# Performance work log

Measured on AMD Instinct MI355X. Metric: run time of the kernel, lower is better.

Reference implementation:

```python
import jax, jax.numpy as jnp
import numpy as np
from jax import lax

NAN_CONV_THRESH = 0.5  # stand-in for os.environ['NAN_CONV_THRESH']
DN = ('NCHW', 'OIHW', 'NCHW')


def nan_conv2d(x, w, stride, padding, groups, thresh):
    """NaN-aware conv: NaN inputs are treated as 0 in the contraction; any
    output window whose NaN fraction exceeds `thresh` is skipped (output NaN)."""
    mask = jnp.isnan(x)
    xf = jnp.where(mask, 0.0, x)
    out = lax.conv_general_dilated(
        xf, w, window_strides=(stride, stride),
        padding=[(padding, padding), (padding, padding)],
        feature_group_count=groups, dimension_numbers=DN)
    cout, cin_g, kh, kw = w.shape
    # per-group NaN count via a ones-kernel conv over the mask
    ones_k = jnp.ones((groups, cin_g, kh, kw), dtype=x.dtype)
    cnt = lax.conv_general_dilated(
        mask.astype(x.dtype), ones_k, window_strides=(stride, stride),
        padding=[(padding, padding), (padding, padding)],
        feature_group_count=groups, dimension_numbers=DN)  # [B, groups, H', W']
    frac = cnt / (cin_g * kh * kw)
    frac = jnp.repeat(frac, cout // groups, axis=1)  # broadcast group frac to out channels
    return jnp.where(frac > thresh, jnp.nan, out)


def setup_inputs() -> dict:
    key = jax.random.key(0)
    k1, k2, k3 = jax.random.split(key, 3)
    B, C, H, W = 4, 128, 256, 256
    Cout, K = 256, 3
    x = jax.random.normal(k1, (B, C, H, W), dtype=jnp.float32)
    w_dw = jax.random.normal(k2, (C, 1, K, K), dtype=jnp.float32) / np.sqrt(K * K)
    w_pw = jax.random.normal(k3, (Cout, C, 1, 1), dtype=jnp.float32) / np.sqrt(C)
    return {"x": x, "w_dw": w_dw, "w_pw": w_pw}


def reference(x, w_dw, w_pw):
    C = x.shape[1]
    y = nan_conv2d(x, w_dw, stride=1, padding=1, groups=C, thresh=NAN_CONV_THRESH)  # depthwise
    y = nan_conv2d(y, w_pw, stride=1, padding=0, groups=1, thresh=NAN_CONV_THRESH)  # pointwise 1x1
    return y
```

## Files before the change

### kernel.cpp

```cpp
#include <hip/hip_runtime.h>
#include <hip/hip_bf16.h>

typedef __attribute__((ext_vector_type(8))) short bf16x8;
typedef __attribute__((ext_vector_type(4))) float f32x4;

#define B    4
#define CIN  128
#define COUT 256
#define H    256
#define W    256
#define HW   (H * W)
#define ROWS 8
#define PXW  64

__device__ __forceinline__ unsigned short f2bf(float f) {
  unsigned int u = __builtin_bit_cast(unsigned int, f);
  u += 0x7fff + ((u >> 16) & 1);
  return (unsigned short)(u >> 16);
}

__global__ void cvt_wpw(const float* __restrict__ w, unsigned short* __restrict__ o) {
  int i = blockIdx.x * 256 + threadIdx.x;
  if (i < COUT * CIN) o[i] = f2bf(w[i]);
}

struct Row { float L; f32x4 a; f32x4 b; float R; };

__device__ __forceinline__ float rget(const Row& r, int j) {
  return (j < 0) ? r.L : (j < 4) ? r.a[j & 3] : (j < 8) ? r.b[j & 3] : r.R;
}

__device__ __forceinline__ Row load_row(const float* xr, int px0, bool pL, bool pR) {
  Row r;
  r.a = *(const f32x4*)(xr + px0);
  r.b = *(const f32x4*)(xr + px0 + 4);
  r.L = pL ? xr[px0 - 1] : 0.f;
  r.R = pR ? xr[px0 + 8] : 0.f;
  return r;
}

__device__ __forceinline__ Row zero_row() {
  Row r; r.L = r.R = 0.f;
  r.a = (f32x4){0.f,0.f,0.f,0.f};
  r.b = (f32x4){0.f,0.f,0.f,0.f};
  return r;
}

__device__ __forceinline__ unsigned swz(unsigned La) {
  unsigned g = ((La >> 8) & 7) ^ ((La >> 11) & 7);
  return La ^ (g << 4);
}

__global__ __launch_bounds__(1024, 4) void fused_kernel(
    const float* __restrict__ x, const float* __restrict__ wdw,
    const unsigned short* __restrict__ wb, float* __restrict__ out)
{
  int bid = blockIdx.x;
  int xcd = bid & 7;
  int k   = bid >> 3;
  int hcl = k & 3;
  int s   = (k >> 2) & 3;
  int b   = k >> 4;
  int hc  = xcd * 4 + hcl;
  int hBase = hc * ROWS;

  int t = threadIdx.x;
  int ci  = t >> 3;
  int pxg = t & 7;
  int px0 = s * PXW + pxg * 8;
  bool pL = px0 > 0, pR = px0 + 8 < W;

  __shared__ __align__(16) char yb[ROWS * PXW * CIN * 2];

  float wr[9];
#pragma unroll
  for (int q = 0; q < 9; ++q) wr[q] = wdw[ci * 9 + q];

  const float* xc = x + ((size_t)b * CIN + ci) * HW;

  Row A  = (hBase > 0) ? load_row(xc + (size_t)(hBase - 1) * W, px0, pL, pR) : zero_row();
  Row Bv = load_row(xc + (size_t)hBase * W, px0, pL, pR);
  Row C  = load_row(xc + (size_t)(hBase + 1) * W, px0, pL, pR);

#pragma unroll
  for (int r = 0; r < ROWS; ++r) {
    Row D;
    if (r < ROWS - 1) {
      int hh = hBase + r + 2;
      bool ok = hh < H;
      D = ok ? load_row(xc + (size_t)hh * W, px0, pL, pR) : zero_row();
    }

#pragma unroll
    for (int j = 0; j < 8; ++j) {
      float a =
        rget(A, j-1)*wr[0] + rget(A, j)*wr[1] + rget(A, j+1)*wr[2] +
        rget(Bv,j-1)*wr[3] + rget(Bv,j)*wr[4] + rget(Bv,j+1)*wr[5] +
        rget(C, j-1)*wr[6] + rget(C, j)*wr[7] + rget(C, j+1)*wr[8];
      unsigned La = (unsigned)r * 16384u + (unsigned)(pxg * 8 + j) * 256u + (unsigned)ci * 2u;
      *(unsigned short*)(yb + swz(La)) = f2bf(a);
    }

    if (r < ROWS - 1) { A = Bv; Bv = C; C = D; }
  }

  int wave = t >> 6, l = t & 63;
  int l15 = l & 15, lg = l >> 4;
  int coBase = wave * 16;

  bf16x8 Af[4];
#pragma unroll
  for (int kk = 0; kk < 4; ++kk)
    Af[kk] = *(const bf16x8*)(wb + (coBase + l15) * CIN + kk * 32 + lg * 8);

  __syncthreads();

  float* ob = out + (size_t)b * COUT * HW + s * PXW;

#pragma unroll
  for (int r = 0; r < ROWS; ++r) {
    f32x4 acc[4];
#pragma unroll
    for (int n = 0; n < 4; ++n) acc[n] = (f32x4){0.f,0.f,0.f,0.f};

#pragma unroll
    for (int n = 0; n < 4; ++n) {
      bf16x8 Bf[4];
#pragma unroll
      for (int kk = 0; kk < 4; ++kk) {
        unsigned La = (unsigned)r * 16384u + (unsigned)(n * 16 + l15) * 256u
                    + (unsigned)(kk * 32 + lg * 8) * 2u;
        Bf[kk] = *(const bf16x8*)(yb + swz(La));
      }
#pragma unroll
      for (int kk = 0; kk < 4; ++kk)
        acc[n] = __builtin_amdgcn_mfma_f32_16x16x32_bf16(Af[kk], Bf[kk], acc[n], 0, 0, 0);
    }

    float* orow = ob + (size_t)(hBase + r) * W;
#pragma unroll
    for (int n = 0; n < 4; ++n)
#pragma unroll
      for (int rr = 0; rr < 4; ++rr)
        orow[(size_t)(coBase + lg * 4 + rr) * HW + n * 16 + l15] = acc[n][rr];
  }
}

extern "C" void kernel_launch(void* const* d_in, const int* in_sizes, int n_in,
                              void* d_out, int out_size, void* d_ws, size_t ws_size,
                              hipStream_t stream) {
  const float* x   = (const float*)d_in[0];
  const float* wdw = (const float*)d_in[1];
  const float* wpw = (const float*)d_in[2];
  float* out = (float*)d_out;

  unsigned short* wbb = (unsigned short*)d_ws;

  cvt_wpw<<<(COUT * CIN + 255) / 256, 256, 0, stream>>>(wpw, wbb);
  fused_kernel<<<B * (H / ROWS) * (W / PXW), 1024, 0, stream>>>(x, wdw, wbb, out);
}
```

Before: 105.0 us.

## Retile fused kernel to full-width 2-row tiles with 2x8 MFMA register blocking

Changes the block tile from 8 rows by 64 pixels to 2 rows by the full 256-pixel width. Each thread now computes 2 channels by 16 pixels in the depthwise stage, and each wave computes a 32-channel by 128-pixel output block, so every B fragment read from LDS feeds two MFMAs. The goal is to cut LDS reads per MFMA and make output row stores fully contiguous. In exchange, halo re-reads rise (4 input rows loaded per 2 output rows instead of 10 per 8), and the larger accumulator array raises register pressure under the 1024-thread, 4-block launch bounds.

```diff
diff --git a/kernel.cpp b/kernel.cpp
--- a/kernel.cpp
+++ b/kernel.cpp
@@ -10,8 +10,8 @@
 #define H    256
 #define W    256
 #define HW   (H * W)
-#define ROWS 8
-#define PXW  64
+#define ROWS 2
+#define PXW  256
 
 __device__ __forceinline__ unsigned short f2bf(float f) {
   unsigned int u = __builtin_bit_cast(unsigned int, f);
@@ -24,25 +24,31 @@
   if (i < COUT * CIN) o[i] = f2bf(w[i]);
 }
 
-struct Row { float L; f32x4 a; f32x4 b; float R; };
+struct R16 { f32x4 v0, v1, v2, v3; float L, R; };
 
-__device__ __forceinline__ float rget(const Row& r, int j) {
-  return (j < 0) ? r.L : (j < 4) ? r.a[j & 3] : (j < 8) ? r.b[j & 3] : r.R;
+__device__ __forceinline__ float rg(const R16& r, int j) {
+  if (j < 0)  return r.L;
+  if (j < 4)  return r.v0[j & 3];
+  if (j < 8)  return r.v1[j & 3];
+  if (j < 12) return r.v2[j & 3];
+  if (j < 16) return r.v3[j & 3];
+  return r.R;
 }
 
-__device__ __forceinline__ Row load_row(const float* xr, int px0, bool pL, bool pR) {
-  Row r;
-  r.a = *(const f32x4*)(xr + px0);
-  r.b = *(const f32x4*)(xr + px0 + 4);
+__device__ __forceinline__ R16 lrow(const float* xr, int px0, bool pL, bool pR) {
+  R16 r;
+  r.v0 = *(const f32x4*)(xr + px0);
+  r.v1 = *(const f32x4*)(xr + px0 + 4);
+  r.v2 = *(const f32x4*)(xr + px0 + 8);
+  r.v3 = *(const f32x4*)(xr + px0 + 12);
   r.L = pL ? xr[px0 - 1] : 0.f;
-  r.R = pR ? xr[px0 + 8] : 0.f;
+  r.R = pR ? xr[px0 + 16] : 0.f;
   return r;
 }
 
-__device__ __forceinline__ Row zero_row() {
-  Row r; r.L = r.R = 0.f;
-  r.a = (f32x4){0.f,0.f,0.f,0.f};
-  r.b = (f32x4){0.f,0.f,0.f,0.f};
+__device__ __forceinline__ R16 zrow() {
+  R16 r; r.L = r.R = 0.f;
+  r.v0 = r.v1 = r.v2 = r.v3 = (f32x4){0.f,0.f,0.f,0.f};
   return r;
 }
 
@@ -57,92 +63,103 @@
 {
   int bid = blockIdx.x;
   int xcd = bid & 7;
-  int k   = bid >> 3;
-  int hcl = k & 3;
-  int s   = (k >> 2) & 3;
-  int b   = k >> 4;
-  int hc  = xcd * 4 + hcl;
+  int q   = bid >> 3;
+  int hcl = q & 15;
+  int b   = q >> 4;
+  int hc  = xcd * 16 + hcl;
   int hBase = hc * ROWS;
 
   int t = threadIdx.x;
-  int ci  = t >> 3;
-  int pxg = t & 7;
-  int px0 = s * PXW + pxg * 8;
-  bool pL = px0 > 0, pR = px0 + 8 < W;
+  int c   = t >> 4;
+  int pxg = t & 15;
+  int ci0 = c * 2;
+  int px0 = pxg * 16;
+  bool pL = px0 > 0, pR = px0 + 16 < W;
 
   __shared__ __align__(16) char yb[ROWS * PXW * CIN * 2];
 
-  float wr[9];
+  float w2[2][9];
 #pragma unroll
-  for (int q = 0; q < 9; ++q) wr[q] = wdw[ci * 9 + q];
-
-  const float* xc = x + ((size_t)b * CIN + ci) * HW;
-
-  Row A  = (hBase > 0) ? load_row(xc + (size_t)(hBase - 1) * W, px0, pL, pR) : zero_row();
-  Row Bv = load_row(xc + (size_t)hBase * W, px0, pL, pR);
-  Row C  = load_row(xc + (size_t)(hBase + 1) * W, px0, pL, pR);
+  for (int cc = 0; cc < 2; ++cc)
+#pragma unroll
+    for (int k = 0; k < 9; ++k) w2[cc][k] = wdw[(ci0 + cc) * 9 + k];
 
 #pragma unroll
-  for (int r = 0; r < ROWS; ++r) {
-    Row D;
-    if (r < ROWS - 1) {
-      int hh = hBase + r + 2;
-      bool ok = hh < H;
-      D = ok ? load_row(xc + (size_t)hh * W, px0, pL, pR) : zero_row();
-    }
+  for (int cc = 0; cc < 2; ++cc) {
+    int ci = ci0 + cc;
+    const float* xc = x + ((size_t)b * CIN + ci) * HW;
+
+    R16 A  = (hBase > 0) ? lrow(xc + (size_t)(hBase - 1) * W, px0, pL, pR) : zrow();
+    R16 Bv = lrow(xc + (size_t)hBase * W, px0, pL, pR);
+    R16 C  = lrow(xc + (size_t)(hBase + 1) * W, px0, pL, pR);
+    R16 D  = (hBase + 2 < H) ? lrow(xc + (size_t)(hBase + 2) * W, px0, pL, pR) : zrow();
 
 #pragma unroll
-    for (int j = 0; j < 8; ++j) {
-      float a =
-        rget(A, j-1)*wr[0] + rget(A, j)*wr[1] + rget(A, j+1)*wr[2] +
-        rget(Bv,j-1)*wr[3] + rget(Bv,j)*wr[4] + rget(Bv,j+1)*wr[5] +
-        rget(C, j-1)*wr[6] + rget(C, j)*wr[7] + rget(C, j+1)*wr[8];
-      unsigned La = (unsigned)r * 16384u + (unsigned)(pxg * 8 + j) * 256u + (unsigned)ci * 2u;
-      *(unsigned short*)(yb + swz(La)) = f2bf(a);
+    for (int r = 0; r < 2; ++r) {
+      const R16& Ra = (r == 0) ? A  : Bv;
+      const R16& Rb = (r == 0) ? Bv : C;
+      const R16& Rc = (r == 0) ? C  : D;
+      const float* wr = w2[cc];
+#pragma unroll
+      for (int j = 0; j < 16; ++j) {
+        float a =
+          rg(Ra,j-1)*wr[0] + rg(Ra,j)*wr[1] + rg(Ra,j+1)*wr[2] +
+          rg(Rb,j-1)*wr[3] + rg(Rb,j)*wr[4] + rg(Rb,j+1)*wr[5] +
+          rg(Rc,j-1)*wr[6] + rg(Rc,j)*wr[7] + rg(Rc,j+1)*wr[8];
+        unsigned La = (unsigned)r * 65536u + (unsigned)(px0 + j) * 256u + (unsigned)ci * 2u;
+        *(unsigned short*)(yb + swz(La)) = f2bf(a);
+      }
     }
-
-    if (r < ROWS - 1) { A = Bv; Bv = C; C = D; }
   }
 
   int wave = t >> 6, l = t & 63;
   int l15 = l & 15, lg = l >> 4;
-  int coBase = wave * 16;
+  int coBase = (wave >> 1) * 32;
+  int pxBase = (wave & 1) * 128;
 
-  bf16x8 Af[4];
+  bf16x8 Af[2][4];
 #pragma unroll
-  for (int kk = 0; kk < 4; ++kk)
-    Af[kk] = *(const bf16x8*)(wb + (coBase + l15) * CIN + kk * 32 + lg * 8);
+  for (int m = 0; m < 2; ++m)
+#pragma unroll
+    for (int kk = 0; kk < 4; ++kk)
+      Af[m][kk] = *(const bf16x8*)(wb + (coBase + m * 16 + l15) * CIN + kk * 32 + lg * 8);
 
   __syncthreads();
 
-  float* ob = out + (size_t)b * COUT * HW + s * PXW;
+  float* ob = out + (size_t)b * COUT * HW;
 
 #pragma unroll
-  for (int r = 0; r < ROWS; ++r) {
-    f32x4 acc[4];
+  for (int r = 0; r < 2; ++r) {
+    f32x4 acc[2][8];
 #pragma unroll
-    for (int n = 0; n < 4; ++n) acc[n] = (f32x4){0.f,0.f,0.f,0.f};
+    for (int m = 0; m < 2; ++m)
+#pragma unroll
+      for (int n = 0; n < 8; ++n) acc[m][n] = (f32x4){0.f,0.f,0.f,0.f};
 
 #pragma unroll
-    for (int n = 0; n < 4; ++n) {
+    for (int n = 0; n < 8; ++n) {
       bf16x8 Bf[4];
 #pragma unroll
       for (int kk = 0; kk < 4; ++kk) {
-        unsigned La = (unsigned)r * 16384u + (unsigned)(n * 16 + l15) * 256u
+        unsigned La = (unsigned)r * 65536u + (unsigned)(pxBase + n * 16 + l15) * 256u
                     + (unsigned)(kk * 32 + lg * 8) * 2u;
         Bf[kk] = *(const bf16x8*)(yb + swz(La));
       }
 #pragma unroll
-      for (int kk = 0; kk < 4; ++kk)
-        acc[n] = __builtin_amdgcn_mfma_f32_16x16x32_bf16(Af[kk], Bf[kk], acc[n], 0, 0, 0);
+      for (int m = 0; m < 2; ++m)
+#pragma unroll
+        for (int kk = 0; kk < 4; ++kk)
+          acc[m][n] = __builtin_amdgcn_mfma_f32_16x16x32_bf16(Af[m][kk], Bf[kk], acc[m][n], 0, 0, 0);
     }
 
     float* orow = ob + (size_t)(hBase + r) * W;
 #pragma unroll
-    for (int n = 0; n < 4; ++n)
+    for (int m = 0; m < 2; ++m)
 #pragma unroll
-      for (int rr = 0; rr < 4; ++rr)
-        orow[(size_t)(coBase + lg * 4 + rr) * HW + n * 16 + l15] = acc[n][rr];
+      for (int n = 0; n < 8; ++n)
+#pragma unroll
+        for (int rr = 0; rr < 4; ++rr)
+          orow[(size_t)(coBase + m * 16 + lg * 4 + rr) * HW + pxBase + n * 16 + l15] = acc[m][n][rr];
   }
 }
 
@@ -157,5 +174,5 @@
   unsigned short* wbb = (unsigned short*)d_ws;
 
   cvt_wpw<<<(COUT * CIN + 255) / 256, 256, 0, stream>>>(wpw, wbb);
-  fused_kernel<<<B * (H / ROWS) * (W / PXW), 1024, 0, stream>>>(x, wdw, wbb, out);
+  fused_kernel<<<B * (H / ROWS), 1024, 0, stream>>>(x, wdw, wbb, out);
 }
```

Result: slower. 132.0 us (+25.7%).

## Reshape block tile to 4 rows by 128 px with 2x register-blocked MFMA

Applied to the files above, without the earlier changes.

Changes the fused depthwise+pointwise block tile from 8 rows by 64 pixels to 4 rows by 128 pixels. Each thread now computes two input channels for the depthwise stage. In the pointwise GEMM each wave covers 32 output channels by 64 pixels, so every B fragment read from LDS feeds two A fragments. The goal is fewer LDS reads per MFMA and longer contiguous output rows, at the cost of more registers, more vertical halo reloads (4-row tiles), and the same LDS footprint.

```diff
diff --git a/kernel.cpp b/kernel.cpp
--- a/kernel.cpp
+++ b/kernel.cpp
@@ -10,8 +10,8 @@
 #define H    256
 #define W    256
 #define HW   (H * W)
-#define ROWS 8
-#define PXW  64
+#define ROWS 4
+#define PXW  128
 
 __device__ __forceinline__ unsigned short f2bf(float f) {
   unsigned int u = __builtin_bit_cast(unsigned int, f);
@@ -58,60 +58,69 @@
   int bid = blockIdx.x;
   int xcd = bid & 7;
   int k   = bid >> 3;
-  int hcl = k & 3;
-  int s   = (k >> 2) & 3;
-  int b   = k >> 4;
-  int hc  = xcd * 4 + hcl;
+  int hcl = k & 7;
+  int sb  = k >> 3;
+  int s   = sb & 1;
+  int b   = sb >> 1;
+  int hc  = xcd * 8 + hcl;
   int hBase = hc * ROWS;
 
   int t = threadIdx.x;
-  int ci  = t >> 3;
-  int pxg = t & 7;
+  int c   = t >> 4;
+  int pxg = t & 15;
+  int ci0 = c * 2;
   int px0 = s * PXW + pxg * 8;
   bool pL = px0 > 0, pR = px0 + 8 < W;
 
   __shared__ __align__(16) char yb[ROWS * PXW * CIN * 2];
 
-  float wr[9];
 #pragma unroll
-  for (int q = 0; q < 9; ++q) wr[q] = wdw[ci * 9 + q];
+  for (int cc = 0; cc < 2; ++cc) {
+    int ci = ci0 + cc;
+    const float* xc = x + ((size_t)b * CIN + ci) * HW;
 
-  const float* xc = x + ((size_t)b * CIN + ci) * HW;
+    float wr[9];
+#pragma unroll
+    for (int q = 0; q < 9; ++q) wr[q] = wdw[ci * 9 + q];
 
-  Row A  = (hBase > 0) ? load_row(xc + (size_t)(hBase - 1) * W, px0, pL, pR) : zero_row();
-  Row Bv = load_row(xc + (size_t)hBase * W, px0, pL, pR);
-  Row C  = load_row(xc + (size_t)(hBase + 1) * W, px0, pL, pR);
+    Row A  = (hBase > 0) ? load_row(xc + (size_t)(hBase - 1) * W, px0, pL, pR) : zero_row();
+    Row Bv = load_row(xc + (size_t)hBase * W, px0, pL, pR);
+    Row C  = load_row(xc + (size_t)(hBase + 1) * W, px0, pL, pR);
 
 #pragma unroll
-  for (int r = 0; r < ROWS; ++r) {
-    Row D;
-    if (r < ROWS - 1) {
-      int hh = hBase + r + 2;
-      bool ok = hh < H;
-      D = ok ? load_row(xc + (size_t)hh * W, px0, pL, pR) : zero_row();
-    }
+    for (int r = 0; r < ROWS; ++r) {
+      Row D;
+      if (r < ROWS - 1) {
+        int hh = hBase + r + 2;
+        bool ok = hh < H;
+        D = ok ? load_row(xc + (size_t)hh * W, px0, pL, pR) : zero_row();
+      }
 
 #pragma unroll
-    for (int j = 0; j < 8; ++j) {
-      float a =
-        rget(A, j-1)*wr[0] + rget(A, j)*wr[1] + rget(A, j+1)*wr[2] +
-        rget(Bv,j-1)*wr[3] + rget(Bv,j)*wr[4] + rget(Bv,j+1)*wr[5] +
-        rget(C, j-1)*wr[6] + rget(C, j)*wr[7] + rget(C, j+1)*wr[8];
-      unsigned La = (unsigned)r * 16384u + (unsigned)(pxg * 8 + j) * 256u + (unsigned)ci * 2u;
-      *(unsigned short*)(yb + swz(La)) = f2bf(a);
+      for (int j = 0; j < 8; ++j) {
+        float a =
+          rget(A, j-1)*wr[0] + rget(A, j)*wr[1] + rget(A, j+1)*wr[2] +
+          rget(Bv,j-1)*wr[3] + rget(Bv,j)*wr[4] + rget(Bv,j+1)*wr[5] +
+          rget(C, j-1)*wr[6] + rget(C, j)*wr[7] + rget(C, j+1)*wr[8];
+        unsigned La = (unsigned)r * 32768u + (unsigned)(pxg * 8 + j) * 256u + (unsigned)ci * 2u;
+        *(unsigned short*)(yb + swz(La)) = f2bf(a);
+      }
+
+      if (r < ROWS - 1) { A = Bv; Bv = C; C = D; }
     }
-
-    if (r < ROWS - 1) { A = Bv; Bv = C; C = D; }
   }
 
   int wave = t >> 6, l = t & 63;
   int l15 = l & 15, lg = l >> 4;
-  int coBase = wave * 16;
+  int coBase = (wave >> 1) * 32;
+  int pxHalf = (wave & 1) * 64;
 
-  bf16x8 Af[4];
+  bf16x8 Af[2][4];
 #pragma unroll
-  for (int kk = 0; kk < 4; ++kk)
-    Af[kk] = *(const bf16x8*)(wb + (coBase + l15) * CIN + kk * 32 + lg * 8);
+  for (int m = 0; m < 2; ++m)
+#pragma unroll
+    for (int kk = 0; kk < 4; ++kk)
+      Af[m][kk] = *(const bf16x8*)(wb + (coBase + m * 16 + l15) * CIN + kk * 32 + lg * 8);
 
   __syncthreads();
 
@@ -119,30 +128,36 @@
 
 #pragma unroll
   for (int r = 0; r < ROWS; ++r) {
-    f32x4 acc[4];
+    f32x4 acc[2][4];
 #pragma unroll
-    for (int n = 0; n < 4; ++n) acc[n] = (f32x4){0.f,0.f,0.f,0.f};
+    for (int m = 0; m < 2; ++m)
+#pragma unroll
+      for (int n = 0; n < 4; ++n) acc[m][n] = (f32x4){0.f,0.f,0.f,0.f};
 
 #pragma unroll
     for (int n = 0; n < 4; ++n) {
       bf16x8 Bf[4];
 #pragma unroll
       for (int kk = 0; kk < 4; ++kk) {
-        unsigned La = (unsigned)r * 16384u + (unsigned)(n * 16 + l15) * 256u
+        unsigned La = (unsigned)r * 32768u + (unsigned)(pxHalf + n * 16 + l15) * 256u
                     + (unsigned)(kk * 32 + lg * 8) * 2u;
         Bf[kk] = *(const bf16x8*)(yb + swz(La));
       }
 #pragma unroll
-      for (int kk = 0; kk < 4; ++kk)
-        acc[n] = __builtin_amdgcn_mfma_f32_16x16x32_bf16(Af[kk], Bf[kk], acc[n], 0, 0, 0);
+      for (int m = 0; m < 2; ++m)
+#pragma unroll
+        for (int kk = 0; kk < 4; ++kk)
+          acc[m][n] = __builtin_amdgcn_mfma_f32_16x16x32_bf16(Af[m][kk], Bf[kk], acc[m][n], 0, 0, 0);
     }
 
     float* orow = ob + (size_t)(hBase + r) * W;
 #pragma unroll
-    for (int n = 0; n < 4; ++n)
+    for (int m = 0; m < 2; ++m)
 #pragma unroll
-      for (int rr = 0; rr < 4; ++rr)
-        orow[(size_t)(coBase + lg * 4 + rr) * HW + n * 16 + l15] = acc[n][rr];
+      for (int n = 0; n < 4; ++n)
+#pragma unroll
+        for (int rr = 0; rr < 4; ++rr)
+          orow[(size_t)(coBase + m * 16 + lg * 4 + rr) * HW + pxHalf + n * 16 + l15] = acc[m][n][rr];
   }
 }
 
```

Result: slower. 107.5 us (+2.3%).

## Double-buffer LDS to overlap depthwise rows with pointwise MFMA GEMM

Applied to the files above, without the earlier changes.

Restructures the fused kernel so the depthwise conv produces two rows at a time into one of two LDS buffers while the MFMA pointwise GEMM consumes the other, with a barrier per pair. LDS use drops from 128KB to 64KB, which may allow more resident blocks. It also swaps the MFMA operand order so each lane holds four consecutive pixels and can write them with one vector store instead of scattered scalar stores. The cost is more barriers and more live registers for the rows loaded ahead.

```diff
diff --git a/kernel.cpp b/kernel.cpp
--- a/kernel.cpp
+++ b/kernel.cpp
@@ -70,7 +70,7 @@
   int px0 = s * PXW + pxg * 8;
   bool pL = px0 > 0, pR = px0 + 8 < W;
 
-  __shared__ __align__(16) char yb[ROWS * PXW * CIN * 2];
+  __shared__ __align__(16) char yb[2 * 32768];
 
   float wr[9];
 #pragma unroll
@@ -78,72 +78,83 @@
 
   const float* xc = x + ((size_t)b * CIN + ci) * HW;
 
-  Row A  = (hBase > 0) ? load_row(xc + (size_t)(hBase - 1) * W, px0, pL, pR) : zero_row();
-  Row Bv = load_row(xc + (size_t)hBase * W, px0, pL, pR);
-  Row C  = load_row(xc + (size_t)(hBase + 1) * W, px0, pL, pR);
-
-#pragma unroll
-  for (int r = 0; r < ROWS; ++r) {
-    Row D;
-    if (r < ROWS - 1) {
-      int hh = hBase + r + 2;
-      bool ok = hh < H;
-      D = ok ? load_row(xc + (size_t)hh * W, px0, pL, pR) : zero_row();
-    }
-
-#pragma unroll
-    for (int j = 0; j < 8; ++j) {
-      float a =
-        rget(A, j-1)*wr[0] + rget(A, j)*wr[1] + rget(A, j+1)*wr[2] +
-        rget(Bv,j-1)*wr[3] + rget(Bv,j)*wr[4] + rget(Bv,j+1)*wr[5] +
-        rget(C, j-1)*wr[6] + rget(C, j)*wr[7] + rget(C, j+1)*wr[8];
-      unsigned La = (unsigned)r * 16384u + (unsigned)(pxg * 8 + j) * 256u + (unsigned)ci * 2u;
-      *(unsigned short*)(yb + swz(La)) = f2bf(a);
-    }
-
-    if (r < ROWS - 1) { A = Bv; Bv = C; C = D; }
-  }
-
   int wave = t >> 6, l = t & 63;
   int l15 = l & 15, lg = l >> 4;
   int coBase = wave * 16;
 
-  bf16x8 Af[4];
+  bf16x8 Wf[4];
 #pragma unroll
   for (int kk = 0; kk < 4; ++kk)
-    Af[kk] = *(const bf16x8*)(wb + (coBase + l15) * CIN + kk * 32 + lg * 8);
+    Wf[kk] = *(const bf16x8*)(wb + (coBase + l15) * CIN + kk * 32 + lg * 8);
 
-  __syncthreads();
+  auto dw_row = [&](char* buf, int rr, const Row& Ra, const Row& Rb, const Row& Rc) {
+#pragma unroll
+    for (int j = 0; j < 8; ++j) {
+      float a =
+        rget(Ra, j-1)*wr[0] + rget(Ra, j)*wr[1] + rget(Ra, j+1)*wr[2] +
+        rget(Rb, j-1)*wr[3] + rget(Rb, j)*wr[4] + rget(Rb, j+1)*wr[5] +
+        rget(Rc, j-1)*wr[6] + rget(Rc, j)*wr[7] + rget(Rc, j+1)*wr[8];
+      unsigned La = (unsigned)rr * 16384u + (unsigned)(pxg * 8 + j) * 256u + (unsigned)ci * 2u;
+      *(unsigned short*)(buf + swz(La)) = f2bf(a);
+    }
+  };
 
-  float* ob = out + (size_t)b * COUT * HW + s * PXW;
+  auto gemm_pair = [&](const char* buf, int p) {
+    float* ob = out + (size_t)b * COUT * HW + s * PXW;
+#pragma unroll
+    for (int rr = 0; rr < 2; ++rr) {
+      int h = hBase + p * 2 + rr;
+      float* orow = ob + (size_t)h * W + (size_t)(coBase + l15) * HW;
+#pragma unroll
+      for (int m = 0; m < 4; ++m) {
+        bf16x8 Yf[4];
+#pragma unroll
+        for (int kk = 0; kk < 4; ++kk) {
+          unsigned La = (unsigned)rr * 16384u + (unsigned)(m * 16 + l15) * 256u
+                      + (unsigned)(kk * 32 + lg * 8) * 2u;
+          Yf[kk] = *(const bf16x8*)(buf + swz(La));
+        }
+        f32x4 acc = (f32x4){0.f,0.f,0.f,0.f};
+#pragma unroll
+        for (int kk = 0; kk < 4; ++kk)
+          acc = __builtin_amdgcn_mfma_f32_16x16x32_bf16(Yf[kk], Wf[kk], acc, 0, 0, 0);
+        *(f32x4*)(orow + m * 16 + lg * 4) = acc;
+      }
+    }
+  };
+
+  Row A  = (hBase > 0) ? load_row(xc + (size_t)(hBase - 1) * W, px0, pL, pR) : zero_row();
+  Row Bv = load_row(xc + (size_t)(hBase + 0) * W, px0, pL, pR);
+  Row C  = load_row(xc + (size_t)(hBase + 1) * W, px0, pL, pR);
+  Row D  = load_row(xc + (size_t)(hBase + 2) * W, px0, pL, pR);
+  Row C2 = load_row(xc + (size_t)(hBase + 3) * W, px0, pL, pR);
+  Row D2 = load_row(xc + (size_t)(hBase + 4) * W, px0, pL, pR);
+
+  dw_row(yb, 0, A, Bv, C);
+  dw_row(yb, 1, Bv, C, D);
+  asm volatile("s_waitcnt lgkmcnt(0)" ::: "memory");
+  __builtin_amdgcn_s_barrier();
 
 #pragma unroll
-  for (int r = 0; r < ROWS; ++r) {
-    f32x4 acc[4];
-#pragma unroll
-    for (int n = 0; n < 4; ++n) acc[n] = (f32x4){0.f,0.f,0.f,0.f};
+  for (int kp = 1; kp < 4; ++kp) {
+    A = C; Bv = D; C = C2; D = D2;
+    if (kp < 3) {
+      int hh = hBase + 2 * kp + 3;
+      bool ok = (hh + 1) < H;
+      C2 = load_row(xc + (size_t)hh * W, px0, pL, pR);
+      D2 = ok ? load_row(xc + (size_t)(hh + 1) * W, px0, pL, pR) : zero_row();
+    }
+    char* wbuf = yb + (kp & 1) * 32768;
+    const char* rbuf = yb + ((kp - 1) & 1) * 32768;
 
-#pragma unroll
-    for (int n = 0; n < 4; ++n) {
-      bf16x8 Bf[4];
-#pragma unroll
-      for (int kk = 0; kk < 4; ++kk) {
-        unsigned La = (unsigned)r * 16384u + (unsigned)(n * 16 + l15) * 256u
-                    + (unsigned)(kk * 32 + lg * 8) * 2u;
-        Bf[kk] = *(const bf16x8*)(yb + swz(La));
-      }
-#pragma unroll
-      for (int kk = 0; kk < 4; ++kk)
-        acc[n] = __builtin_amdgcn_mfma_f32_16x16x32_bf16(Af[kk], Bf[kk], acc[n], 0, 0, 0);
-    }
+    gemm_pair(rbuf, kp - 1);
+    dw_row(wbuf, 0, A, Bv, C);
+    dw_row(wbuf, 1, Bv, C, D);
+    asm volatile("s_waitcnt lgkmcnt(0)" ::: "memory");
+    __builtin_amdgcn_s_barrier();
+  }
 
-    float* orow = ob + (size_t)(hBase + r) * W;
-#pragma unroll
-    for (int n = 0; n < 4; ++n)
-#pragma unroll
-      for (int rr = 0; rr < 4; ++rr)
-        orow[(size_t)(coBase + lg * 4 + rr) * HW + n * 16 + l15] = acc[n][rr];
-  }
+  gemm_pair(yb + 32768, 3);
 }
 
 extern "C" void kernel_launch(void* const* d_in, const int* in_sizes, int n_in,
```

Measured after the change: 155.3 us. 47.9% more time.
